# Performance work log

Hardware: AMD Instinct MI355X
Metric: run time of the kernel (lower is better)

Reference implementation:

```python
import jax, jax.numpy as jnp
import numpy as np

N_NODES = 100000
N_EDGES = 1000000
N_QUERY = 100000
F_IN = 64
HIDDEN = 64
LABEL_DIM = 2


def setup_inputs() -> dict:
    key = jax.random.key(0)
    ks = jax.random.split(key, 16)
    inp = {}
    for i, nm in enumerate(["Xr", "Xi", "Xj", "Xk"]):
        inp[nm] = jax.random.normal(ks[i], (N_NODES, F_IN), dtype=jnp.float32)
    for i, nm in enumerate(["norm_r", "norm_i", "norm_j", "norm_k"]):
        inp[nm] = jax.random.normal(ks[4 + i], (N_EDGES,), dtype=jnp.float32) * 0.1
    inp["edge_index"] = jax.random.randint(ks[8], (2, N_EDGES), 0, N_NODES)
    inp["query_edges"] = jax.random.randint(ks[9], (N_QUERY, 2), 0, N_NODES)
    s1 = (2.0 / (F_IN + HIDDEN)) ** 0.5  # glorot
    inp["W1"] = jax.random.normal(ks[10], (4, F_IN, HIDDEN), dtype=jnp.float32) * s1
    inp["b1"] = jnp.zeros((4, HIDDEN), dtype=jnp.float32)
    s2 = (2.0 / (HIDDEN + HIDDEN)) ** 0.5
    inp["W2"] = jax.random.normal(ks[11], (4, HIDDEN, HIDDEN), dtype=jnp.float32) * s2
    inp["b2"] = jnp.zeros((4, HIDDEN), dtype=jnp.float32)
    inp["Cw"] = jax.random.normal(ks[12], (LABEL_DIM, 8 * HIDDEN), dtype=jnp.float32) * 0.05
    inp["Cb"] = jnp.zeros((LABEL_DIM,), dtype=jnp.float32)
    return inp


def _quaconv(Xs, src, dst, norms, W, b, n_nodes):
    # Xs: list of 4 [N,F] components; norms: list of 4 [E] Laplacian norms.
    # P[a][b] = propagate(X_a, -norm_b) = scatter_add over dst of (-norm_b)_e * X_a[src_e]
    P = []
    for a in range(4):
        G = Xs[a][src]  # [E, F] gather, reused for all 4 norms
        P.append([jax.ops.segment_sum((-norms[b])[:, None] * G, dst, num_segments=n_nodes)
                  for b in range(4)])
    Tr = P[0][0] - P[1][1] - P[2][2] - P[3][3]
    Ti = P[1][0] + P[0][1] + P[3][2] - P[2][3]
    Tj = P[2][0] - P[3][1] + P[0][2] + P[1][3]
    Tk = P[3][0] + P[2][1] - P[1][2] + P[0][3]
    Wr, Wi, Wj, Wk = W[0], W[1], W[2], W[3]
    out_r = Tr @ Wr - Ti @ Wi - Tj @ Wj - Tk @ Wk + b[0]
    out_i = Tr @ Wi + Ti @ Wr + Tj @ Wk - Tk @ Wj + b[1]
    out_j = Tr @ Wj - Ti @ Wk + Tj @ Wr + Tk @ Wi + b[2]
    out_k = Tr @ Wk + Ti @ Wj - Tj @ Wi + Tk @ Wr + b[3]
    return out_r, out_i, out_j, out_k


def _forward(Xr, Xi, Xj, Xk, norm_r, norm_i, norm_j, norm_k,
             W1, b1, W2, b2, Cw, Cb, edge_index, query_edges):
    src, dst = edge_index[0], edge_index[1]
    n = Xr.shape[0]
    norms = [norm_r, norm_i, norm_j, norm_k]
    Xs = [Xr, Xi, Xj, Xk]
    for W, b in ((W1, b1), (W2, b2)):
        Xs = list(_quaconv(Xs, src, dst, norms, W, b, n))
        # complex_relu_layer_different: mask = 1.0*(x>=0); mask*x == relu(x)
        Xs = [jax.nn.relu(x) for x in Xs]
    q0, q1 = query_edges[:, 0], query_edges[:, 1]
    # cat(real[q0], real[q1], imag_i[q0], imag_i[q1], ...) -> [Eq, 8*hidden]
    feats = jnp.concatenate([c[idx] for c in Xs for idx in (q0, q1)], axis=-1)
    # dropout is identity at inference; Conv1d(kernel=1) == linear over channels
    logits = feats @ Cw.T + Cb  # [Eq, label_dim]
    return jax.nn.log_softmax(logits, axis=-1)


def reference(Xr, Xi, Xj, Xk, norm_r, norm_i, norm_j, norm_k,
              W1, b1, W2, b2, Cw, Cb, edge_index, query_edges):
    return _forward(Xr, Xi, Xj, Xk, norm_r, norm_i, norm_j, norm_k,
                    W1, b1, W2, b2, Cw, Cb, edge_index, query_edges)
```

## Files before the change

kernel.cpp:

```cpp
#include <hip/hip_runtime.h>
#include <hip/hip_bf16.h>

#define N_NODESC 100000
#define N_EDGESC 1000000
#define N_QUERYC 100000

typedef short short8 __attribute__((ext_vector_type(8)));
typedef short s16x2 __attribute__((ext_vector_type(2)));
typedef float f32x4 __attribute__((ext_vector_type(4)));

__device__ __forceinline__ float ldf(const void* p, int i, int isbf) {
  return isbf ? __bfloat162float(((const __hip_bfloat16*)p)[i])
              : ((const float*)p)[i];
}
__device__ __forceinline__ unsigned short f2b(float x) {
  __hip_bfloat16 h = __float2bfloat16(x);
  return *(unsigned short*)&h;
}
__device__ __forceinline__ float b2f(unsigned int u) {
  return __uint_as_float(u << 16);
}
__device__ __forceinline__ s16x2 u2s(unsigned u) {
  union { unsigned u; s16x2 s; } c; c.u = u; return c.s;
}
__device__ __forceinline__ void gload16(const void* g, void* l) {
  __builtin_amdgcn_global_load_lds(
      (const __attribute__((address_space(1))) void*)g,
      (__attribute__((address_space(3))) void*)l, 16, 0, 0);
}

__global__ void k_prep(const void* x, int* flag, int* cnt, int n) {
  int bid = blockIdx.x;
  int t = threadIdx.x;
  if (bid == 0) {
    __shared__ int scnt;
    if (t == 0) scnt = 0;
    __syncthreads();
    const unsigned short* h = (const unsigned short*)x;
    int local = 0;
    for (int i = t; i < 4096; i += 256) {
      int e = (h[i] >> 7) & 0xFF;
      if (e >= 107 && e <= 133) local++;
    }
    atomicAdd(&scnt, local);
    __syncthreads();
    if (t == 0) *flag = (scnt >= 3482) ? 1 : 0;
  } else {
    int i = (bid - 1) * 256 + t;
    if (i < n) cnt[i] = 0;
  }
}

__global__ __launch_bounds__(256) void k_hist_ilv(
    const int* __restrict__ ei, int* __restrict__ cnt, int ne, int histBlocks,
    const void* X0, const void* X1, const void* X2, const void* X3,
    const int* __restrict__ flagp, unsigned short* __restrict__ Xg, int n) {
  int bid = blockIdx.x;
  if (bid < histBlocks) {
    int e = bid * 256 + threadIdx.x;
    if (e < ne) atomicAdd(&cnt[ei[ne + e]], 1);
  } else {
    int isbf = *flagp;
    int lane = threadIdx.x & 63;
    int node = (bid - histBlocks) * 4 + (threadIdx.x >> 6);
    if (node >= n) return;
    int idx = node * 64 + lane;
    unsigned int lo = f2b(ldf(X0, idx, isbf)) | ((unsigned int)f2b(ldf(X1, idx, isbf)) << 16);
    unsigned int hi = f2b(ldf(X2, idx, isbf)) | ((unsigned int)f2b(ldf(X3, idx, isbf)) << 16);
    uint2 g = make_uint2(lo, hi);
    *(uint2*)(Xg + (size_t)node * 256 + lane * 4) = g;
  }
}

__global__ void k_scan1(const int* __restrict__ cnt, int* __restrict__ off,
                        int* __restrict__ partials, int n) {
  __shared__ int s[1024];
  int t = threadIdx.x;
  int idx = blockIdx.x * 1024 + t;
  int v = (idx < n) ? cnt[idx] : 0;
  s[t] = v;
  __syncthreads();
  for (int d = 1; d < 1024; d <<= 1) {
    int tmp = (t >= d) ? s[t - d] : 0;
    __syncthreads();
    s[t] += tmp;
    __syncthreads();
  }
  if (idx < n) off[idx] = s[t] - v;
  if (t == 1023) partials[blockIdx.x] = s[1023];
}

__global__ void k_scan2(const int* __restrict__ partials, int* __restrict__ pref,
                        int* __restrict__ off, int nb, int npos) {
  __shared__ int s[128];
  int t = threadIdx.x;
  int v = (t < nb) ? partials[t] : 0;
  s[t] = v;
  __syncthreads();
  for (int d = 1; d < 128; d <<= 1) {
    int tmp = (t >= d) ? s[t - d] : 0;
    __syncthreads();
    s[t] += tmp;
    __syncthreads();
  }
  if (t < nb) pref[t] = s[t] - v;
  if (t == 127) off[npos] = s[127];
}

__global__ void k_scan3(int* __restrict__ off, const int* __restrict__ pref,
                        int* __restrict__ cursor, int n) {
  int i = blockIdx.x * 256 + threadIdx.x;
  if (i < n) {
    int o = off[i] + pref[i >> 10];
    off[i] = o;
    cursor[i] = o;
  }
}

__global__ void k_fill(const int* __restrict__ ei,
                       const void* nr, const void* ni, const void* nj, const void* nk,
                       const int* __restrict__ flagp, int* __restrict__ cursor,
                       uint4* __restrict__ recs, int ne) {
  int isbf = *flagp;
  int e = blockIdx.x * 256 + threadIdx.x;
  if (e >= ne) return;
  int s = ei[e];
  int d = ei[ne + e];
  int pos = atomicAdd(&cursor[d], 1);
  uint4 r;
  r.x = (unsigned)s;
  r.y = (unsigned)f2b(-ldf(nr, e, isbf)) | ((unsigned)f2b(-ldf(ni, e, isbf)) << 16);
  r.z = (unsigned)f2b(-ldf(nj, e, isbf)) | ((unsigned)f2b(-ldf(nk, e, isbf)) << 16);
  r.w = 0;
  recs[pos] = r;
}

#if __has_builtin(__builtin_amdgcn_fdot2_f32_bf16)
#define USE_DOT2 1
#else
#define USE_DOT2 0
#endif
__global__ __launch_bounds__(128, 8) void k_agg(
    const unsigned short* __restrict__ Xg, const int* __restrict__ off,
    const uint4* __restrict__ recs, unsigned short* __restrict__ Tf, int nnodes) {
  __shared__ unsigned short tl4[2][4][256];
  int lane = threadIdx.x & 63;
  int w = threadIdx.x >> 6;
  int gq = blockIdx.x * 2 + w;
  int n0 = gq * 4;
  if (n0 >= nnodes) return;

  int o_[5];
#pragma unroll
  for (int i = 0; i < 5; i++) o_[i] = __builtin_amdgcn_readfirstlane(off[n0 + i]);

#pragma unroll
  for (int n = 0; n < 4; ++n) {
    int rs = o_[n], re = o_[n + 1];
    float tr = 0.f, ti = 0.f, tj = 0.f, tk = 0.f;

    auto qacc = [&](uint2 g, unsigned mx, unsigned my) {
#if USE_DOT2
      unsigned a = mx, b = my;
      unsigned sa = (a >> 16) | (a << 16);
      unsigned sb = (b >> 16) | (b << 16);
      unsigned A1 = a ^ 0x80000000u;
      unsigned A2 = b ^ 0x80008000u;
      unsigned B2 = sb ^ 0x00008000u;
      unsigned D2 = sb ^ 0x80000000u;
      s16x2 gx = u2s(g.x), gy = u2s(g.y);
      tr = __builtin_amdgcn_fdot2_f32_bf16(u2s(A1), gx, tr, false);
      tr = __builtin_amdgcn_fdot2_f32_bf16(u2s(A2), gy, tr, false);
      ti = __builtin_amdgcn_fdot2_f32_bf16(u2s(sa), gx, ti, false);
      ti = __builtin_amdgcn_fdot2_f32_bf16(u2s(B2), gy, ti, false);
      tj = __builtin_amdgcn_fdot2_f32_bf16(u2s(b),  gx, tj, false);
      tj = __builtin_amdgcn_fdot2_f32_bf16(u2s(A1), gy, tj, false);
      tk = __builtin_amdgcn_fdot2_f32_bf16(u2s(D2), gx, tk, false);
      tk = __builtin_amdgcn_fdot2_f32_bf16(u2s(sa), gy, tk, false);
#else
      float mr = __uint_as_float(mx << 16), mi = __uint_as_float(mx & 0xffff0000u);
      float mj = __uint_as_float(my << 16), mk = __uint_as_float(my & 0xffff0000u);
      float xr = __uint_as_float(g.x << 16), xi = __uint_as_float(g.x & 0xffff0000u);
      float xj = __uint_as_float(g.y << 16), xk = __uint_as_float(g.y & 0xffff0000u);
      tr += mr * xr - mi * xi - mj * xj - mk * xk;
      ti += mr * xi + mi * xr + mj * xk - mk * xj;
      tj += mr * xj - mi * xk + mj * xr + mk * xi;
      tk += mr * xk + mi * xj - mj * xi + mk * xr;
#endif
    };

    int e = rs;
    for (; e + 8 <= re; e += 8) {
      uint4 r[8];
#pragma unroll
      for (int u = 0; u < 8; u++) r[u] = recs[e + u];
      int ss[8];
      unsigned sx[8], sy[8];
#pragma unroll
      for (int u = 0; u < 8; u++) {
        ss[u] = __builtin_amdgcn_readfirstlane((int)r[u].x);
        sx[u] = __builtin_amdgcn_readfirstlane(r[u].y);
        sy[u] = __builtin_amdgcn_readfirstlane(r[u].z);
      }
      uint2 g[8];
#pragma unroll
      for (int u = 0; u < 8; u++)
        g[u] = *(const uint2*)(Xg + (size_t)ss[u] * 256 + lane * 4);
#pragma unroll
      for (int u = 0; u < 8; u++) qacc(g[u], sx[u], sy[u]);
    }
    for (; e < re; ++e) {
      uint4 r = recs[e];
      int s = __builtin_amdgcn_readfirstlane((int)r.x);
      unsigned mx = __builtin_amdgcn_readfirstlane(r.y);
      unsigned my = __builtin_amdgcn_readfirstlane(r.z);
      uint2 g0 = *(const uint2*)(Xg + (size_t)s * 256 + lane * 4);
      qacc(g0, mx, my);
    }

    tl4[w][n][lane] = f2b(tr);
    tl4[w][n][64 + lane] = f2b(ti);
    tl4[w][n][128 + lane] = f2b(tj);
    tl4[w][n][192 + lane] = f2b(tk);
  }
  __builtin_amdgcn_wave_barrier();

  size_t blk = (size_t)(gq >> 2) * 4096;
  int qi = gq & 3;
#pragma unroll
  for (int h = 0; h < 2; ++h) {
    int m = h * 64 + lane;
    int n = m & 3, l = m >> 2;
    uint4 v = *(const uint4*)&tl4[w][n][l * 8];
    size_t o = blk + (size_t)(l >> 2) * 512 + (l & 3) * 128 + qi * 32 + n * 8;
    *(uint4*)(Tf + o) = v;
  }
}

__global__ void k_weff2(const void* W1, const void* b1, const void* W2, const void* b2,
                        const int* __restrict__ flagp,
                        unsigned short* __restrict__ Wq1, float* __restrict__ bcat1,
                        unsigned short* __restrict__ Wq2, float* __restrict__ bcat2) {
  int isbf = *flagp;
  int layer = blockIdx.x >> 6;
  const void* W = layer ? W2 : W1;
  const void* b = layer ? b2 : b1;
  unsigned short* Wq = layer ? Wq2 : Wq1;
  float* bcat = layer ? bcat2 : bcat1;
  int t = (blockIdx.x & 63) * 256 + threadIdx.x;
  int w4 = t >> 12;
  int h = (t >> 6) & 63;
  int kk = t & 63;
  int s = (kk >> 3) ^ (h & 7);
  Wq[(w4 * 64 + h) * 64 + s * 8 + (kk & 7)] = f2b(ldf(W, w4 * 4096 + kk * 64 + h, isbf));
  if (t < 256) bcat[t] = ldf(b, t, isbf);
}

__global__ __launch_bounds__(256, 2) void k_gemm(
    const unsigned short* __restrict__ A, const unsigned short* __restrict__ Wq,
    const float* __restrict__ bias, int M, int mode,
    unsigned short* __restrict__ XgOut,
    float* __restrict__ P1, float* __restrict__ P2,
    const void* Cw, const int* __restrict__ flagp) {
  __shared__ unsigned short Wsm[16384];

  int t = threadIdx.x;
  int lane = t & 63;
  int w = t >> 6;
  int l15 = lane & 15, quad = lane >> 4;
  int m0 = blockIdx.x * 64;
  int hh = (w & 1) * 32;

#pragma unroll
  for (int i = 0; i < 8; i++)
    gload16((const char*)Wq + (size_t)(i * 256 + t) * 16,
            (char*)Wsm + (size_t)(i * 256 + w * 64) * 16);
  __syncthreads();

  short8 av[2][8];
  int n16 = blockIdx.x * 4 + (w >> 1) * 2;
#pragma unroll
  for (int mi = 0; mi < 2; mi++)
#pragma unroll
    for (int kc = 0; kc < 8; kc++)
      av[mi][kc] = *(const short8*)(A + (size_t)(n16 + mi) * 4096 + kc * 512 + lane * 8);

  f32x4 acc[2][4][2];
#pragma unroll
  for (int mi = 0; mi < 2; mi++)
#pragma unroll
    for (int c = 0; c < 4; c++)
#pragma unroll
      for (int hb = 0; hb < 2; hb++) acc[mi][c][hb] = (f32x4){0.f, 0.f, 0.f, 0.f};

#pragma unroll
  for (int kc = 0; kc < 8; kc++) {
    int a = kc >> 1;
    short8 bv[4][2];
#pragma unroll
    for (int c = 0; c < 4; c++) {
      int w4 = a ^ c;
      int neg = (0x3950 >> (a * 4 + c)) & 1;
#pragma unroll
      for (int hb = 0; hb < 2; hb++) {
        int h = hh + hb * 16 + l15;
        int lc = ((kc & 1) * 4 + quad) ^ (l15 & 7);
        short8 bb = *(const short8*)&Wsm[(w4 * 64 + h) * 64 + lc * 8];
        if (neg) {
          uint4 u = *(uint4*)&bb;
          u.x ^= 0x80008000u; u.y ^= 0x80008000u;
          u.z ^= 0x80008000u; u.w ^= 0x80008000u;
          bb = *(short8*)&u;
        }
        bv[c][hb] = bb;
      }
    }
#pragma unroll
    for (int mi = 0; mi < 2; mi++)
#pragma unroll
      for (int c = 0; c < 4; c++)
#pragma unroll
        for (int hb = 0; hb < 2; hb++)
          acc[mi][c][hb] =
              __builtin_amdgcn_mfma_f32_16x16x32_bf16(av[mi][kc], bv[c][hb], acc[mi][c][hb], 0, 0, 0);
  }

  float bias_v[4][2];
#pragma unroll
  for (int c = 0; c < 4; c++)
#pragma unroll
    for (int hb = 0; hb < 2; hb++) bias_v[c][hb] = bias[c * 64 + hh + hb * 16 + l15];

  if (mode == 0) {
#pragma unroll
    for (int mi = 0; mi < 2; mi++) {
#pragma unroll
      for (int hb = 0; hb < 2; hb++) {
#pragma unroll
        for (int r = 0; r < 4; r++) {
          int node = m0 + (w >> 1) * 32 + mi * 16 + quad * 4 + r;
          unsigned int lo =
              f2b(fmaxf(acc[mi][0][hb][r] + bias_v[0][hb], 0.f)) |
              ((unsigned int)f2b(fmaxf(acc[mi][1][hb][r] + bias_v[1][hb], 0.f)) << 16);
          unsigned int hi =
              f2b(fmaxf(acc[mi][2][hb][r] + bias_v[2][hb], 0.f)) |
              ((unsigned int)f2b(fmaxf(acc[mi][3][hb][r] + bias_v[3][hb], 0.f)) << 16);
          *(uint2*)(XgOut + (size_t)node * 256 + (hh + hb * 16 + l15) * 4) =
              make_uint2(lo, hi);
        }
      }
    }
  } else {
    int isbf = *flagp;
    float cw[4][2][4];
#pragma unroll
    for (int c = 0; c < 4; c++)
#pragma unroll
      for (int hb = 0; hb < 2; hb++) {
        int h = hh + hb * 16 + l15;
#pragma unroll
        for (int d = 0; d < 2; d++)
#pragma unroll
          for (int e = 0; e < 2; e++)
            cw[c][hb][e + 2 * d] = ldf(Cw, d * 512 + c * 128 + e * 64 + h, isbf);
      }
    float* Pout = (hh == 0) ? P1 : P2;
#pragma unroll
    for (int mi = 0; mi < 2; mi++) {
#pragma unroll
      for (int r = 0; r < 4; r++) {
        int node = m0 + (w >> 1) * 32 + mi * 16 + quad * 4 + r;
        float pd0 = 0.f, pd1 = 0.f, pd2 = 0.f, pd3 = 0.f;
#pragma unroll
        for (int c = 0; c < 4; c++)
#pragma unroll
          for (int hb = 0; hb < 2; hb++) {
            float v = fmaxf(acc[mi][c][hb][r] + bias_v[c][hb], 0.f);
            pd0 += v * cw[c][hb][0];
            pd1 += v * cw[c][hb][1];
            pd2 += v * cw[c][hb][2];
            pd3 += v * cw[c][hb][3];
          }
#pragma unroll
        for (int o = 1; o < 16; o <<= 1) {
          pd0 += __shfl_xor(pd0, o);
          pd1 += __shfl_xor(pd1, o);
          pd2 += __shfl_xor(pd2, o);
          pd3 += __shfl_xor(pd3, o);
        }
        if (l15 == 0 && node < M) {
          f32x4 st = {pd0, pd1, pd2, pd3};
          *(f32x4*)(Pout + (size_t)node * 4) = st;
        }
      }
    }
  }
}

__global__ void k_query(const int* __restrict__ qe,
                        const float* __restrict__ P1, const float* __restrict__ P2,
                        const void* Cb, const int* __restrict__ flagp,
                        void* out, int nq) {
  int isbf = *flagp;
  int q = blockIdx.x * 256 + threadIdx.x;
  if (q >= nq) return;
  int q0 = qe[q * 2], q1 = qe[q * 2 + 1];
  f32x4 a0 = *(const f32x4*)(P1 + (size_t)q0 * 4);
  f32x4 b0 = *(const f32x4*)(P2 + (size_t)q0 * 4);
  f32x4 a1 = *(const f32x4*)(P1 + (size_t)q1 * 4);
  f32x4 b1 = *(const f32x4*)(P2 + (size_t)q1 * 4);
  float l0 = (a0[0] + b0[0]) + (a1[1] + b1[1]) + ldf(Cb, 0, isbf);
  float l1 = (a0[2] + b0[2]) + (a1[3] + b1[3]) + ldf(Cb, 1, isbf);
  float m = fmaxf(l0, l1);
  float lse = m + logf(expf(l0 - m) + expf(l1 - m));
  float o0 = l0 - lse, o1 = l1 - lse;
  if (isbf) {
    __hip_bfloat16* o = (__hip_bfloat16*)out;
    o[q * 2] = __float2bfloat16(o0);
    o[q * 2 + 1] = __float2bfloat16(o1);
  } else {
    float* o = (float*)out;
    o[q * 2] = o0;
    o[q * 2 + 1] = o1;
  }
}

extern "C" void kernel_launch(void* const* d_in, const int* in_sizes, int n_in,
                              void* d_out, int out_size, void* d_ws, size_t ws_size,
                              hipStream_t stream) {
  const int N = N_NODESC, NE = N_EDGESC, NQ = N_QUERYC;
  const int NPAD = 100224;

  char* w = (char*)d_ws;
  auto alloc = [&](size_t bytes) -> void* {
    void* p = (void*)w;
    w += (bytes + 255) & ~(size_t)255;
    return p;
  };
  int* flag       = (int*)alloc(4);
  int* offsets    = (int*)alloc((size_t)(N + 1) * 4);
  int* cursor     = (int*)alloc((size_t)N * 4);
  int* partials   = (int*)alloc(128 * 4);
  int* pref       = (int*)alloc(128 * 4);
  uint4* recs     = (uint4*)alloc((size_t)NE * 16);
  unsigned short* Tf = (unsigned short*)alloc((size_t)NPAD * 256 * 2);
  unsigned short* Xg = (unsigned short*)alloc((size_t)NPAD * 256 * 2);
  unsigned short* Wq1 = (unsigned short*)alloc(16384 * 2);
  unsigned short* Wq2 = (unsigned short*)alloc(16384 * 2);
  float* bcat1    = (float*)alloc(256 * 4);
  float* bcat2    = (float*)alloc(256 * 4);
  float* P1       = (float*)alloc((size_t)N * 4 * 4);
  float* P2       = (float*)alloc((size_t)N * 4 * 4);
  (void)ws_size; (void)n_in; (void)in_sizes; (void)out_size;

  const int* ei = (const int*)d_in[8];

  k_prep<<<392, 256, 0, stream>>>(d_in[0], flag, cursor, N);

  k_weff2<<<128, 256, 0, stream>>>(d_in[10], d_in[11], d_in[12], d_in[13], flag,
                                   Wq1, bcat1, Wq2, bcat2);

  int histBlocks = (NE + 255) / 256;
  int ilvBlocks = (N + 3) / 4;
  k_hist_ilv<<<histBlocks + ilvBlocks, 256, 0, stream>>>(
      ei, cursor, NE, histBlocks,
      d_in[0], d_in[1], d_in[2], d_in[3], flag, Xg, N);

  k_scan1<<<(N + 1023) / 1024, 1024, 0, stream>>>(cursor, offsets, partials, N);
  k_scan2<<<1, 128, 0, stream>>>(partials, pref, offsets, (N + 1023) / 1024, N);
  k_scan3<<<(N + 255) / 256, 256, 0, stream>>>(offsets, pref, cursor, N);
  k_fill<<<(NE + 255) / 256, 256, 0, stream>>>(ei, d_in[4], d_in[5], d_in[6], d_in[7],
                                               flag, cursor, recs, NE);

  int ggrid = (N + 63) / 64;
  int nquads = (N + 3) / 4;
  int agrid = (nquads + 1) / 2;

  k_agg<<<agrid, 128, 0, stream>>>(Xg, offsets, recs, Tf, N);
  k_gemm<<<ggrid, 256, 0, stream>>>(Tf, Wq1, bcat1, N, 0, Xg, nullptr, nullptr,
                                    nullptr, flag);

  k_agg<<<agrid, 128, 0, stream>>>(Xg, offsets, recs, Tf, N);
  k_gemm<<<ggrid, 256, 0, stream>>>(Tf, Wq2, bcat2, N, 1, nullptr, P1, P2,
                                    d_in[14], flag);

  k_query<<<(NQ + 255) / 256, 256, 0, stream>>>((const int*)d_in[9], P1, P2,
                                                d_in[15], flag, d_out, NQ);
}
```

Measured before the change: 509.1 us.

## Fuse histogram with record build, pad counters, interleave query partials

The CSR build now takes each edge's slot within its destination during the histogram pass itself, with the atomic on a padded counter array so neighbouring counters sit on separate cache lines. It writes the packed edge record with that slot into a temp buffer that reuses the Tf storage. A lightweight scatter kernel then places each record at offset plus slot, which removes the second atomic pass over the cursor array. The two per-node partial-logit arrays are merged into one interleaved array so each query endpoint reads one contiguous 32-byte span. In exchange it adds a temp round trip through memory and an eight-times larger counter array to clear.

```diff
diff --git a/kernel.cpp b/kernel.cpp
--- a/kernel.cpp
+++ b/kernel.cpp
@@ -4,6 +4,7 @@
 #define N_NODESC 100000
 #define N_EDGESC 1000000
 #define N_QUERYC 100000
+#define CNT_STRIDE 8
 
 typedef short short8 __attribute__((ext_vector_type(8)));
 typedef short s16x2 __attribute__((ext_vector_type(2)));
@@ -29,7 +30,7 @@
       (__attribute__((address_space(3))) void*)l, 16, 0, 0);
 }
 
-__global__ void k_prep(const void* x, int* flag, int* cnt, int n) {
+__global__ void k_prep(const void* x, int* flag, int* cnt, int nc) {
   int bid = blockIdx.x;
   int t = threadIdx.x;
   if (bid == 0) {
@@ -47,22 +48,34 @@
     if (t == 0) *flag = (scnt >= 3482) ? 1 : 0;
   } else {
     int i = (bid - 1) * 256 + t;
-    if (i < n) cnt[i] = 0;
-  }
-}
-
-__global__ __launch_bounds__(256) void k_hist_ilv(
-    const int* __restrict__ ei, int* __restrict__ cnt, int ne, int histBlocks,
+    if (i < nc) cnt[i] = 0;
+  }
+}
+
+__global__ __launch_bounds__(256) void k_fill0_ilv(
+    const int* __restrict__ ei,
+    const void* nr, const void* ni, const void* nj, const void* nk,
+    int* __restrict__ cnt, uint4* __restrict__ temp, int ne, int fillBlocks,
     const void* X0, const void* X1, const void* X2, const void* X3,
     const int* __restrict__ flagp, unsigned short* __restrict__ Xg, int n) {
   int bid = blockIdx.x;
-  if (bid < histBlocks) {
+  if (bid < fillBlocks) {
+    int isbf = *flagp;
     int e = bid * 256 + threadIdx.x;
-    if (e < ne) atomicAdd(&cnt[ei[ne + e]], 1);
+    if (e >= ne) return;
+    int s = ei[e];
+    int d = ei[ne + e];
+    int pos = atomicAdd(&cnt[d * CNT_STRIDE], 1);
+    uint4 r;
+    r.x = (unsigned)s;
+    r.y = (unsigned)f2b(-ldf(nr, e, isbf)) | ((unsigned)f2b(-ldf(ni, e, isbf)) << 16);
+    r.z = (unsigned)f2b(-ldf(nj, e, isbf)) | ((unsigned)f2b(-ldf(nk, e, isbf)) << 16);
+    r.w = (unsigned)pos;
+    temp[e] = r;
   } else {
     int isbf = *flagp;
     int lane = threadIdx.x & 63;
-    int node = (bid - histBlocks) * 4 + (threadIdx.x >> 6);
+    int node = (bid - fillBlocks) * 4 + (threadIdx.x >> 6);
     if (node >= n) return;
     int idx = node * 64 + lane;
     unsigned int lo = f2b(ldf(X0, idx, isbf)) | ((unsigned int)f2b(ldf(X1, idx, isbf)) << 16);
@@ -77,7 +90,7 @@
   __shared__ int s[1024];
   int t = threadIdx.x;
   int idx = blockIdx.x * 1024 + t;
-  int v = (idx < n) ? cnt[idx] : 0;
+  int v = (idx < n) ? cnt[idx * CNT_STRIDE] : 0;
   s[t] = v;
   __syncthreads();
   for (int d = 1; d < 1024; d <<= 1) {
@@ -107,32 +120,19 @@
   if (t == 127) off[npos] = s[127];
 }
 
-__global__ void k_scan3(int* __restrict__ off, const int* __restrict__ pref,
-                        int* __restrict__ cursor, int n) {
+__global__ void k_scan3(int* __restrict__ off, const int* __restrict__ pref, int n) {
   int i = blockIdx.x * 256 + threadIdx.x;
-  if (i < n) {
-    int o = off[i] + pref[i >> 10];
-    off[i] = o;
-    cursor[i] = o;
-  }
-}
-
-__global__ void k_fill(const int* __restrict__ ei,
-                       const void* nr, const void* ni, const void* nj, const void* nk,
-                       const int* __restrict__ flagp, int* __restrict__ cursor,
-                       uint4* __restrict__ recs, int ne) {
-  int isbf = *flagp;
+  if (i < n) off[i] = off[i] + pref[i >> 10];
+}
+
+__global__ void k_scatter(const int* __restrict__ ei, const uint4* __restrict__ temp,
+                          const int* __restrict__ off, uint4* __restrict__ recs, int ne) {
   int e = blockIdx.x * 256 + threadIdx.x;
   if (e >= ne) return;
-  int s = ei[e];
+  uint4 r = temp[e];
   int d = ei[ne + e];
-  int pos = atomicAdd(&cursor[d], 1);
-  uint4 r;
-  r.x = (unsigned)s;
-  r.y = (unsigned)f2b(-ldf(nr, e, isbf)) | ((unsigned)f2b(-ldf(ni, e, isbf)) << 16);
-  r.z = (unsigned)f2b(-ldf(nj, e, isbf)) | ((unsigned)f2b(-ldf(nk, e, isbf)) << 16);
-  r.w = 0;
-  recs[pos] = r;
+  int pos = (int)r.w;
+  recs[off[d] + pos] = r;
 }
 
 #if __has_builtin(__builtin_amdgcn_fdot2_f32_bf16)
@@ -260,8 +260,7 @@
     const unsigned short* __restrict__ A, const unsigned short* __restrict__ Wq,
     const float* __restrict__ bias, int M, int mode,
     unsigned short* __restrict__ XgOut,
-    float* __restrict__ P1, float* __restrict__ P2,
-    const void* Cw, const int* __restrict__ flagp) {
+    float* __restrict__ P, const void* Cw, const int* __restrict__ flagp) {
   __shared__ unsigned short Wsm[16384];
 
   int t = threadIdx.x;
@@ -364,7 +363,7 @@
           for (int e = 0; e < 2; e++)
             cw[c][hb][e + 2 * d] = ldf(Cw, d * 512 + c * 128 + e * 64 + h, isbf);
       }
-    float* Pout = (hh == 0) ? P1 : P2;
+    float* Pout = P + ((hh == 0) ? 0 : 4);
 #pragma unroll
     for (int mi = 0; mi < 2; mi++) {
 #pragma unroll
@@ -390,25 +389,24 @@
         }
         if (l15 == 0 && node < M) {
           f32x4 st = {pd0, pd1, pd2, pd3};
-          *(f32x4*)(Pout + (size_t)node * 4) = st;
+          *(f32x4*)(Pout + (size_t)node * 8) = st;
         }
       }
     }
   }
 }
 
-__global__ void k_query(const int* __restrict__ qe,
-                        const float* __restrict__ P1, const float* __restrict__ P2,
+__global__ void k_query(const int* __restrict__ qe, const float* __restrict__ P,
                         const void* Cb, const int* __restrict__ flagp,
                         void* out, int nq) {
   int isbf = *flagp;
   int q = blockIdx.x * 256 + threadIdx.x;
   if (q >= nq) return;
   int q0 = qe[q * 2], q1 = qe[q * 2 + 1];
-  f32x4 a0 = *(const f32x4*)(P1 + (size_t)q0 * 4);
-  f32x4 b0 = *(const f32x4*)(P2 + (size_t)q0 * 4);
-  f32x4 a1 = *(const f32x4*)(P1 + (size_t)q1 * 4);
-  f32x4 b1 = *(const f32x4*)(P2 + (size_t)q1 * 4);
+  f32x4 a0 = *(const f32x4*)(P + (size_t)q0 * 8);
+  f32x4 b0 = *(const f32x4*)(P + (size_t)q0 * 8 + 4);
+  f32x4 a1 = *(const f32x4*)(P + (size_t)q1 * 8);
+  f32x4 b1 = *(const f32x4*)(P + (size_t)q1 * 8 + 4);
   float l0 = (a0[0] + b0[0]) + (a1[1] + b1[1]) + ldf(Cb, 0, isbf);
   float l1 = (a0[2] + b0[2]) + (a1[3] + b1[3]) + ldf(Cb, 1, isbf);
   float m = fmaxf(l0, l1);
@@ -439,7 +437,7 @@
   };
   int* flag       = (int*)alloc(4);
   int* offsets    = (int*)alloc((size_t)(N + 1) * 4);
-  int* cursor     = (int*)alloc((size_t)N * 4);
+  int* cnt        = (int*)alloc((size_t)N * CNT_STRIDE * 4);
   int* partials   = (int*)alloc(128 * 4);
   int* pref       = (int*)alloc(128 * 4);
   uint4* recs     = (uint4*)alloc((size_t)NE * 16);
@@ -449,41 +447,39 @@
   unsigned short* Wq2 = (unsigned short*)alloc(16384 * 2);
   float* bcat1    = (float*)alloc(256 * 4);
   float* bcat2    = (float*)alloc(256 * 4);
-  float* P1       = (float*)alloc((size_t)N * 4 * 4);
-  float* P2       = (float*)alloc((size_t)N * 4 * 4);
+  float* P        = (float*)alloc((size_t)N * 8 * 4);
+  uint4* temp     = (uint4*)Tf;
   (void)ws_size; (void)n_in; (void)in_sizes; (void)out_size;
 
   const int* ei = (const int*)d_in[8];
 
-  k_prep<<<392, 256, 0, stream>>>(d_in[0], flag, cursor, N);
+  int nc = N * CNT_STRIDE;
+  k_prep<<<1 + (nc + 255) / 256, 256, 0, stream>>>(d_in[0], flag, cnt, nc);
 
   k_weff2<<<128, 256, 0, stream>>>(d_in[10], d_in[11], d_in[12], d_in[13], flag,
                                    Wq1, bcat1, Wq2, bcat2);
 
-  int histBlocks = (NE + 255) / 256;
+  int fillBlocks = (NE + 255) / 256;
   int ilvBlocks = (N + 3) / 4;
-  k_hist_ilv<<<histBlocks + ilvBlocks, 256, 0, stream>>>(
-      ei, cursor, NE, histBlocks,
+  k_fill0_ilv<<<fillBlocks + ilvBlocks, 256, 0, stream>>>(
+      ei, d_in[4], d_in[5], d_in[6], d_in[7], cnt, temp, NE, fillBlocks,
       d_in[0], d_in[1], d_in[2], d_in[3], flag, Xg, N);
 
-  k_scan1<<<(N + 1023) / 1024, 1024, 0, stream>>>(cursor, offsets, partials, N);
+  k_scan1<<<(N + 1023) / 1024, 1024, 0, stream>>>(cnt, offsets, partials, N);
   k_scan2<<<1, 128, 0, stream>>>(partials, pref, offsets, (N + 1023) / 1024, N);
-  k_scan3<<<(N + 255) / 256, 256, 0, stream>>>(offsets, pref, cursor, N);
-  k_fill<<<(NE + 255) / 256, 256, 0, stream>>>(ei, d_in[4], d_in[5], d_in[6], d_in[7],
-                                               flag, cursor, recs, NE);
+  k_scan3<<<(N + 255) / 256, 256, 0, stream>>>(offsets, pref, N);
+  k_scatter<<<fillBlocks, 256, 0, stream>>>(ei, temp, offsets, recs, NE);
 
   int ggrid = (N + 63) / 64;
   int nquads = (N + 3) / 4;
   int agrid = (nquads + 1) / 2;
 
   k_agg<<<agrid, 128, 0, stream>>>(Xg, offsets, recs, Tf, N);
-  k_gemm<<<ggrid, 256, 0, stream>>>(Tf, Wq1, bcat1, N, 0, Xg, nullptr, nullptr,
-                                    nullptr, flag);
+  k_gemm<<<ggrid, 256, 0, stream>>>(Tf, Wq1, bcat1, N, 0, Xg, nullptr, nullptr, flag);
 
   k_agg<<<agrid, 128, 0, stream>>>(Xg, offsets, recs, Tf, N);
-  k_gemm<<<ggrid, 256, 0, stream>>>(Tf, Wq2, bcat2, N, 1, nullptr, P1, P2,
-                                    d_in[14], flag);
-
-  k_query<<<(NQ + 255) / 256, 256, 0, stream>>>((const int*)d_in[9], P1, P2,
-                                                d_in[15], flag, d_out, NQ);
-}
+  k_gemm<<<ggrid, 256, 0, stream>>>(Tf, Wq2, bcat2, N, 1, nullptr, P, d_in[14], flag);
+
+  k_query<<<(NQ + 255) / 256, 256, 0, stream>>>((const int*)d_in[9], P, d_in[15],
+                                                flag, d_out, NQ);
+}
```

Measured after the change: 467.1 us. 1.09x faster.
